# Optimization experiments

Hardware: AMD Instinct MI355X
Metric: run time of the kernel (lower is better)

The kernel has to match this reference:

```python
import jax, jax.numpy as jnp
import numpy as np

Y = 1      # init kwarg y
DIM = 2    # init kwarg dim


def setup_inputs() -> dict:
    key = jax.random.key(0)
    k1, k2, k3 = jax.random.split(key, 3)
    B, L = 16, 512
    H = 32
    x = jax.random.normal(k1, (B, L, L), dtype=jnp.float32)
    # xavier_uniform-like init for weights
    lim1 = np.sqrt(6.0 / (3 + H)).astype(np.float32)
    W1 = jax.random.uniform(k2, (H, 3), dtype=jnp.float32, minval=-lim1, maxval=lim1)
    b1 = jnp.zeros((H,), dtype=jnp.float32)
    lim2 = np.sqrt(6.0 / (H + 1)).astype(np.float32)
    W2 = jax.random.uniform(k3, (1, H), dtype=jnp.float32, minval=-lim2, maxval=lim2)
    b2 = jnp.zeros((1,), dtype=jnp.float32)
    return {"x": x, "W1": W1, "b1": b1, "W2": W2, "b2": b2}


def reference(x, W1, b1, W2, b2):
    # nearest-neighbor sum along both lattice dims
    x1 = (jnp.roll(x, 1, axis=1) + jnp.roll(x, -1, axis=1)
          + jnp.roll(x, 1, axis=2) + jnp.roll(x, -1, axis=2))
    # shifted-by-y neighbor sum along DIM
    sx = jnp.roll(x, Y, axis=DIM) + jnp.roll(x, -Y, axis=DIM)
    # per-site 3-feature vector: [x^2, x1*x, sx*x] -> (B, L, L, 3)
    inp = jnp.stack([x * x, x1 * x, sx * x], axis=-1)
    # tiny pointwise MLP 3 -> 32 -> 1
    h = jnp.tanh(jnp.einsum('blmf,hf->blmh', inp, W1) + b1)
    out = jnp.einsum('blmh,oh->blmo', h, W2)[..., 0] + b2[0]
    # sum over lattice sites -> per-config scalar (B,)
    return out.sum(axis=(1, 2))
```

## Files before the change

### kernel.cpp

```cpp
#include <hip/hip_runtime.h>

#define L 512
#define LMASK 511
#define HID 32

constexpr int THREADS        = 256;
constexpr int ROWS_PER_BLOCK = 4;
constexpr int BLOCKS_PER_B   = L / ROWS_PER_BLOCK;
constexpr int NTAB           = 2048;
constexpr int GT             = 5;
constexpr int NPAIR_E        = 6;

constexpr float MAGIC   = 8388608.0f;
constexpr float CLAMPLO = 8388608.0f;
constexpr float CLAMPHI = 8396796.0f;

__global__ __launch_bounds__(THREADS)
void site_kernel(const float* __restrict__ x,
                 const float* __restrict__ W1,
                 const float* __restrict__ b1,
                 const float* __restrict__ W2,
                 float* __restrict__ partial) {
    __shared__ __align__(16) float tab_s[NTAB];
    __shared__ __align__(16) float zw_s[GT * 16];
    __shared__ __align__(16) float w2t_s[GT * 4];
    __shared__ __align__(16) float ew_s[NPAIR_E * 8];
    __shared__ __align__(8)  float ew2_s[NPAIR_E * 2];

    const int t = threadIdx.x;
    const float Ke = 2.8853900817779268f;

    if (t < HID) {
        if (t < 4 * GT) {
            const float K256 = 256.0f * Ke;
            const int g = t >> 2, q = t & 3;
            zw_s[g * 16 +  0 + q] = K256 * W1[t * 3 + 0];
            zw_s[g * 16 +  4 + q] = K256 * W1[t * 3 + 1];
            zw_s[g * 16 +  8 + q] = K256 * W1[t * 3 + 2];
            zw_s[g * 16 + 12 + q] = fmaf(K256, b1[t], 4098.0f + MAGIC);
            w2t_s[t] = -2.0f * W2[t];
        } else {
            const int e = t - 4 * GT, p = e >> 1, q = e & 1;
            ew_s[p * 8 + 0 + q] = Ke * W1[t * 3 + 0];
            ew_s[p * 8 + 2 + q] = Ke * W1[t * 3 + 1];
            ew_s[p * 8 + 4 + q] = Ke * W1[t * 3 + 2];
            ew_s[p * 8 + 6 + q] = Ke * b1[t];
            ew2_s[p * 2 + q]    = -2.0f * W2[t];
        }
    }
    for (int i = t; i < NTAB; i += THREADS) {
        const float zp = fmaf((float)i, 0.015625f, -16.001953125f);
        tab_s[i] = __builtin_amdgcn_rcpf(1.0f + __builtin_amdgcn_exp2f(zp));
    }
    __syncthreads();

    const int blk = blockIdx.x;
    const int b   = blk >> 7;
    const int i0  = (blk & (BLOCKS_PER_B - 1)) * ROWS_PER_BLOCK;
    const float* __restrict__ xb = x + (size_t)b * (L * L);

    float F0[8], F1[8], F2[8];
#pragma unroll
    for (int g = 0; g < 2; ++g) {
        const int j  = t + g * THREADS;
        const int jm = (j + LMASK) & LMASK, jp = (j + 1) & LMASK;

        float cc[6];
#pragma unroll
        for (int r = 0; r < 6; ++r) {
            const int i = (i0 + r - 1 + L) & LMASK;
            cc[r] = xb[i * L + j];
        }
#pragma unroll
        for (int s = 0; s < 4; ++s) {
            const int i   = i0 + s;
            const float lf = xb[i * L + jm];
            const float rg = xb[i * L + jp];
            const float c  = cc[s + 1];
            const float lr = lf + rg;
            const float x1 = lr + cc[s] + cc[s + 2];
            const int k = g * 4 + s;
            F0[k] = c * c;  F1[k] = x1 * c;  F2[k] = lr * c;
        }
    }

    float acc[8] = {0.f, 0.f, 0.f, 0.f, 0.f, 0.f, 0.f, 0.f};
    const char* __restrict__ tb = (const char*)tab_s;

    auto tgroup = [&](const int gq) {
        const float4 wa  = *(const float4*)&zw_s[gq * 16 + 0];
        const float4 wb  = *(const float4*)&zw_s[gq * 16 + 4];
        const float4 wc  = *(const float4*)&zw_s[gq * 16 + 8];
        const float4 w0  = *(const float4*)&zw_s[gq * 16 + 12];
        const float4 w2v = *(const float4*)&w2t_s[gq * 4];
#pragma unroll
        for (int q = 0; q < 4; ++q) {
            const float waq = ((const float*)&wa)[q];
            const float wbq = ((const float*)&wb)[q];
            const float wcq = ((const float*)&wc)[q];
            const float w0q = ((const float*)&w0)[q];
            const float w2q = ((const float*)&w2v)[q];
#pragma unroll
            for (int s = 0; s < 8; ++s) {
                const float uu = fmaf(F0[s], waq, fmaf(F1[s], wbq, fmaf(F2[s], wcq, w0q)));
                const float uc = __builtin_amdgcn_fmed3f(uu, CLAMPLO, CLAMPHI);
                const int  off = __float_as_int(uc) & 0x007FFFFC;
                const float y  = *reinterpret_cast<const float*>(tb + off);
                acc[s] = fmaf(w2q, y, acc[s]);
            }
        }
    };
    auto epair = [&](const int p) {
        const float4 e0 = *(const float4*)&ew_s[p * 8 + 0];
        const float4 e1 = *(const float4*)&ew_s[p * 8 + 4];
        const float2 w2p = *(const float2*)&ew2_s[p * 2];
        const float wa0 = e0.x, wa1 = e0.y, wb0 = e0.z, wb1 = e0.w;
        const float wc0 = e1.x, wc1 = e1.y, w00 = e1.z, w01 = e1.w;
#pragma unroll
        for (int s = 0; s < 8; ++s) {
            float z0 = fmaf(F0[s], wa0, fmaf(F1[s], wb0, fmaf(F2[s], wc0, w00)));
            float z1 = fmaf(F0[s], wa1, fmaf(F1[s], wb1, fmaf(F2[s], wc1, w01)));
            z0 = __builtin_amdgcn_fmed3f(z0, -30.0f, 30.0f);
            z1 = __builtin_amdgcn_fmed3f(z1, -30.0f, 30.0f);
            const float d0 = 1.0f + __builtin_amdgcn_exp2f(z0);
            const float d1 = 1.0f + __builtin_amdgcn_exp2f(z1);
            const float nm = fmaf(w2p.x, d1, w2p.y * d0);
            const float rr = __builtin_amdgcn_rcpf(d0 * d1);
            acc[s] = fmaf(nm, rr, acc[s]);
        }
    };

    tgroup(0); epair(0);
    tgroup(1); epair(1);
    tgroup(2); epair(2);
    tgroup(3); epair(3);
    tgroup(4); epair(4); epair(5);

    float a = ((acc[0] + acc[1]) + (acc[2] + acc[3]))
            + ((acc[4] + acc[5]) + (acc[6] + acc[7]));
#pragma unroll
    for (int off = 32; off > 0; off >>= 1)
        a += __shfl_down(a, off, 64);

    __shared__ float wsum[THREADS / 64];
    const int wid = t >> 6, lane = t & 63;
    if (lane == 0) wsum[wid] = a;
    __syncthreads();
    if (t == 0)
        partial[blk] = (wsum[0] + wsum[1]) + (wsum[2] + wsum[3]);
}

__global__ __launch_bounds__(128)
void reduce_kernel(const float* __restrict__ partial,
                   const float* __restrict__ W2,
                   const float* __restrict__ b2,
                   float* __restrict__ out) {
    const int b = blockIdx.x, t = threadIdx.x;
    const float NS = (float)(L * L);

    float v = partial[b * BLOCKS_PER_B + t];
    if (t < HID) v += NS * W2[t];
    if (t == 0)  v += NS * b2[0];

#pragma unroll
    for (int off = 32; off > 0; off >>= 1)
        v += __shfl_down(v, off, 64);

    __shared__ float ws2[2];
    if ((t & 63) == 0) ws2[t >> 6] = v;
    __syncthreads();
    if (t == 0) out[b] = ws2[0] + ws2[1];
}

extern "C" void kernel_launch(void* const* d_in, const int* in_sizes, int n_in,
                              void* d_out, int out_size, void* d_ws, size_t ws_size,
                              hipStream_t stream) {
    const float* x  = (const float*)d_in[0];
    const float* W1 = (const float*)d_in[1];
    const float* b1 = (const float*)d_in[2];
    const float* W2 = (const float*)d_in[3];
    const float* b2 = (const float*)d_in[4];
    float* out      = (float*)d_out;
    float* partial  = (float*)d_ws;

    const int B = in_sizes[0] / (L * L);

    site_kernel<<<B * BLOCKS_PER_B, THREADS, 0, stream>>>(x, W1, b1, W2, partial);
    reduce_kernel<<<B, 128, 0, stream>>>(partial, W2, b2, out);
}
```

Measured before the change: 32.28 us.

## Fuse final reduction into site kernel via last-block atomic and widen tanh table

Removes the separate reduce kernel: each block increments a global counter and the last block sums all partials and writes the outputs, with a memset to reset the counter. The tanh lookup table doubles in size to cover a wider argument range, so the fmed3 clamp is dropped and the index is masked directly. The exact-evaluation pairs also lose their clamp. Out-of-range arguments now wrap around the table instead of saturating, and the final reduction runs serially in one block, with its hardcoded loop covering 16 batches.

```diff
diff --git a/kernel.cpp b/kernel.cpp
--- a/kernel.cpp
+++ b/kernel.cpp
@@ -7,20 +7,22 @@
 constexpr int THREADS        = 256;
 constexpr int ROWS_PER_BLOCK = 4;
 constexpr int BLOCKS_PER_B   = L / ROWS_PER_BLOCK;
-constexpr int NTAB           = 2048;
+constexpr int NTAB           = 4096;
 constexpr int GT             = 5;
 constexpr int NPAIR_E        = 6;
 
-constexpr float MAGIC   = 8388608.0f;
-constexpr float CLAMPLO = 8388608.0f;
-constexpr float CLAMPHI = 8396796.0f;
+constexpr float MAGIC = 8388608.0f;
+constexpr float BIASB = 8194.0f;
 
 __global__ __launch_bounds__(THREADS)
 void site_kernel(const float* __restrict__ x,
                  const float* __restrict__ W1,
                  const float* __restrict__ b1,
                  const float* __restrict__ W2,
-                 float* __restrict__ partial) {
+                 const float* __restrict__ b2,
+                 float* __restrict__ partial,
+                 int*   __restrict__ cnt,
+                 float* __restrict__ out) {
     __shared__ __align__(16) float tab_s[NTAB];
     __shared__ __align__(16) float zw_s[GT * 16];
     __shared__ __align__(16) float w2t_s[GT * 4];
@@ -37,7 +39,7 @@
             zw_s[g * 16 +  0 + q] = K256 * W1[t * 3 + 0];
             zw_s[g * 16 +  4 + q] = K256 * W1[t * 3 + 1];
             zw_s[g * 16 +  8 + q] = K256 * W1[t * 3 + 2];
-            zw_s[g * 16 + 12 + q] = fmaf(K256, b1[t], 4098.0f + MAGIC);
+            zw_s[g * 16 + 12 + q] = fmaf(K256, b1[t], BIASB + MAGIC);
             w2t_s[t] = -2.0f * W2[t];
         } else {
             const int e = t - 4 * GT, p = e >> 1, q = e & 1;
@@ -49,7 +51,7 @@
         }
     }
     for (int i = t; i < NTAB; i += THREADS) {
-        const float zp = fmaf((float)i, 0.015625f, -16.001953125f);
+        const float zp = fmaf((float)i, 0.015625f, -32.001953125f);
         tab_s[i] = __builtin_amdgcn_rcpf(1.0f + __builtin_amdgcn_exp2f(zp));
     }
     __syncthreads();
@@ -103,8 +105,7 @@
 #pragma unroll
             for (int s = 0; s < 8; ++s) {
                 const float uu = fmaf(F0[s], waq, fmaf(F1[s], wbq, fmaf(F2[s], wcq, w0q)));
-                const float uc = __builtin_amdgcn_fmed3f(uu, CLAMPLO, CLAMPHI);
-                const int  off = __float_as_int(uc) & 0x007FFFFC;
+                const int  off = __float_as_int(uu) & 0x3FFC;
                 const float y  = *reinterpret_cast<const float*>(tb + off);
                 acc[s] = fmaf(w2q, y, acc[s]);
             }
@@ -118,10 +119,8 @@
         const float wc0 = e1.x, wc1 = e1.y, w00 = e1.z, w01 = e1.w;
 #pragma unroll
         for (int s = 0; s < 8; ++s) {
-            float z0 = fmaf(F0[s], wa0, fmaf(F1[s], wb0, fmaf(F2[s], wc0, w00)));
-            float z1 = fmaf(F0[s], wa1, fmaf(F1[s], wb1, fmaf(F2[s], wc1, w01)));
-            z0 = __builtin_amdgcn_fmed3f(z0, -30.0f, 30.0f);
-            z1 = __builtin_amdgcn_fmed3f(z1, -30.0f, 30.0f);
+            const float z0 = fmaf(F0[s], wa0, fmaf(F1[s], wb0, fmaf(F2[s], wc0, w00)));
+            const float z1 = fmaf(F0[s], wa1, fmaf(F1[s], wb1, fmaf(F2[s], wc1, w01)));
             const float d0 = 1.0f + __builtin_amdgcn_exp2f(z0);
             const float d1 = 1.0f + __builtin_amdgcn_exp2f(z1);
             const float nm = fmaf(w2p.x, d1, w2p.y * d0);
@@ -143,33 +142,33 @@
         a += __shfl_down(a, off, 64);
 
     __shared__ float wsum[THREADS / 64];
+    __shared__ int   last_s;
     const int wid = t >> 6, lane = t & 63;
     if (lane == 0) wsum[wid] = a;
     __syncthreads();
-    if (t == 0)
+    if (t == 0) {
         partial[blk] = (wsum[0] + wsum[1]) + (wsum[2] + wsum[3]);
-}
+        __threadfence();
+        const int old = atomicAdd(cnt, 1);
+        last_s = (old == (int)gridDim.x - 1);
+    }
+    __syncthreads();
+    if (!last_s) return;
 
-__global__ __launch_bounds__(128)
-void reduce_kernel(const float* __restrict__ partial,
-                   const float* __restrict__ W2,
-                   const float* __restrict__ b2,
-                   float* __restrict__ out) {
-    const int b = blockIdx.x, t = threadIdx.x;
-    const float NS = (float)(L * L);
-
-    float v = partial[b * BLOCKS_PER_B + t];
-    if (t < HID) v += NS * W2[t];
-    if (t == 0)  v += NS * b2[0];
-
+    __threadfence();
+    const int cb = t >> 4, k = t & 15;
+    const float* pb = partial + cb * BLOCKS_PER_B + k * 8;
+    float v = 0.0f;
 #pragma unroll
-    for (int off = 32; off > 0; off >>= 1)
-        v += __shfl_down(v, off, 64);
-
-    __shared__ float ws2[2];
-    if ((t & 63) == 0) ws2[t >> 6] = v;
-    __syncthreads();
-    if (t == 0) out[b] = ws2[0] + ws2[1];
+    for (int i = 0; i < 8; ++i) v += pb[i];
+#pragma unroll
+    for (int off = 8; off > 0; off >>= 1)
+        v += __shfl_down(v, off, 16);
+    if (k == 0) {
+        float cw = b2[0];
+        for (int h = 0; h < HID; ++h) cw += W2[h];
+        out[cb] = v + 262144.0f * cw;
+    }
 }
 
 extern "C" void kernel_launch(void* const* d_in, const int* in_sizes, int n_in,
@@ -182,9 +181,11 @@
     const float* b2 = (const float*)d_in[4];
     float* out      = (float*)d_out;
     float* partial  = (float*)d_ws;
+    int*   cnt      = (int*)(partial + 2048);
 
     const int B = in_sizes[0] / (L * L);
 
-    site_kernel<<<B * BLOCKS_PER_B, THREADS, 0, stream>>>(x, W1, b1, W2, partial);
-    reduce_kernel<<<B, 128, 0, stream>>>(partial, W2, b2, out);
+    hipMemsetAsync(cnt, 0, sizeof(int), stream);
+    site_kernel<<<B * BLOCKS_PER_B, THREADS, 0, stream>>>(
+        x, W1, b1, W2, b2, partial, cnt, out);
 }
```

Measured after the change: 59.38 us. +84.0%, slower.
